# Kernel optimization log

Hardware: AMD Instinct MI355X
Metric: run time of the kernel (lower is better)

Reference implementation:

```python
import jax, jax.numpy as jnp
import numpy as np

B, C_IN, H, W = 32, 128, 64, 64
C_OUT, KH, KW = 256, 3, 3


def setup_inputs() -> dict:
    key = jax.random.key(0)
    k1, k2, k3 = jax.random.split(key, 3)
    inputs = jax.random.normal(k1, (B, C_IN, H, W), dtype=jnp.float32)
    weights = jax.random.normal(k2, (C_OUT, C_IN, KH, KW), dtype=jnp.float32) * 0.05
    bias = jax.random.normal(k3, (C_OUT, 1), dtype=jnp.float32)
    return {"inputs": inputs, "weights": weights, "bias": bias}


def reference(inputs, weights, bias):
    # Direct 2D valid convolution, stride 1, padding 0 (module default).
    # output[b,o,i,j] = sum_{c,u,v} inputs[b,c,i+u,j+v] * weights[o,c,u,v] + bias[o]
    out = jax.lax.conv_general_dilated(
        inputs, weights,
        window_strides=(1, 1),
        padding="VALID",
        dimension_numbers=("NCHW", "OIHW", "NCHW"),
    )
    # bias has shape (C_out, 1); broadcast per output channel
    return out + bias.reshape(1, -1, 1, 1)
```

## Files before the change

kernel.cpp:

```cpp
#include <hip/hip_runtime.h>
#include <hip/hip_bf16.h>
#include <stdint.h>

#define BB   32
#define CIN  128
#define HH   64
#define WW   64
#define COUT 256
#define OHH  62
#define OWW  62
#define PIX_PER_B (OHH*OWW)
#define NPIX (BB*PIX_PER_B)
#define KTOT (9*CIN)

typedef __bf16 bf16x8 __attribute__((ext_vector_type(8)));
typedef float  f32x4  __attribute__((ext_vector_type(4)));
typedef uint16_t u16x8 __attribute__((ext_vector_type(8)));

__device__ __forceinline__ uint16_t f2bf(float f) {
    uint32_t u = __float_as_uint(f);
    uint32_t r = (u + 0x7FFFu + ((u >> 16) & 1u)) >> 16;
    return (uint16_t)r;
}

__device__ __forceinline__ void gload_lds16(const void* g, void* l) {
    __builtin_amdgcn_global_load_lds(
        (const __attribute__((address_space(1))) uint32_t*)g,
        (__attribute__((address_space(3))) uint32_t*)l, 16, 0, 0);
}

__global__ void __launch_bounds__(256) to_nhwc(const float* __restrict__ in,
                                               uint16_t* __restrict__ out) {
    int slab = blockIdx.x;
    int b = slab >> 6, h = slab & 63;
    int w  = threadIdx.x & 63;
    int cp = threadIdx.x >> 6;
    const float* src = in + (((size_t)b * CIN) * HH + h) * WW + w;
    uint16_t* dst = out + ((size_t)slab * WW + w) * CIN;
    #pragma unroll
    for (int it = 0; it < 4; ++it) {
        int c0 = cp * 32 + it * 8;
        u16x8 v;
        #pragma unroll
        for (int j = 0; j < 8; ++j) v[j] = f2bf(src[(c0 + j) * (HH * WW)]);
        *reinterpret_cast<u16x8*>(dst + c0) = v;
    }
}

__global__ void __launch_bounds__(256) pack_w(const float* __restrict__ w,
                                              uint16_t* __restrict__ out) {
    int idx = blockIdx.x * 256 + threadIdx.x;
    int o = idx / KTOT;
    int k = idx - o * KTOT;
    int uv = k >> 7, c = k & 127;
    out[idx] = f2bf(w[(o * CIN + c) * 9 + uv]);
}

__global__ void __launch_bounds__(256) conv_mfma(
        const uint16_t* __restrict__ Xg,
        const uint16_t* __restrict__ Wg,
        const float*    __restrict__ bias,
        float*          __restrict__ out)
{
    __shared__ char lds[32 * 1024 + 1024];
    char* Alds = lds;
    char* Xlds = lds + 16 * 1024;
    int*  pbase = (int*)(lds + 32 * 1024);
    int*  obase = (int*)(lds + 32 * 1024 + 512);

    const int tid  = threadIdx.x;
    const int lane = tid & 63;
    const int wid  = tid >> 6;
    const int bid  = blockIdx.x;
    const int mt = bid & 1;
    const int nt = bid >> 1;

    if (tid < 128) {
        int n  = nt * 128 + tid;
        int b  = n / PIX_PER_B;
        int rem = n - b * PIX_PER_B;
        int oh = rem / OWW;
        int ow = rem - oh * OWW;
        pbase[tid] = ((b * 64 + oh) * 64 + ow) * 128;
        obase[tid] = b * (COUT * PIX_PER_B) + rem;
    }
    __syncthreads();

    const int kc = ((lane & 7) ^ ((lane >> 3) & 7)) * 16;
    int xrow_off[4];
    int arow_off[4];
    #pragma unroll
    for (int q = 0; q < 4; ++q) {
        int t   = wid * 4 + q;
        int row = t * 8 + (lane >> 3);
        xrow_off[q] = pbase[row];
        arow_off[q] = (mt * 128 + row) * KTOT;
    }

    f32x4 acc[4][4] = {};
    const char* XgB = (const char*)Xg;
    const char* WgB = (const char*)Wg;
    const int wm = wid >> 1, wn = wid & 1;

    for (int uv = 0; uv < 9; ++uv) {
        int u = uv / 3, v = uv - u * 3;
        int ioff = (u * 64 + v) * 128;
        #pragma unroll
        for (int ch = 0; ch < 2; ++ch) {
            int c0   = ch * 64;
            int koff = uv * 128 + c0;
            #pragma unroll
            for (int q = 0; q < 4; ++q) {
                int t = wid * 4 + q;
                gload_lds16(WgB + 2 * (arow_off[q] + koff) + kc,
                            Alds + t * 1024 + lane * 16);
                gload_lds16(XgB + 2 * (xrow_off[q] + ioff + c0) + kc,
                            Xlds + t * 1024 + lane * 16);
            }
            __syncthreads();
            #pragma unroll
            for (int ks = 0; ks < 2; ++ks) {
                bf16x8 af[4], xf[4];
                #pragma unroll
                for (int mi = 0; mi < 4; ++mi) {
                    int row = wm * 64 + mi * 16 + (lane & 15);
                    int by  = row * 128 +
                              ((ks * 64 + (lane >> 4) * 16) ^ ((row & 7) << 4));
                    af[mi] = *reinterpret_cast<const bf16x8*>(Alds + by);
                }
                #pragma unroll
                for (int nj = 0; nj < 4; ++nj) {
                    int row = wn * 64 + nj * 16 + (lane & 15);
                    int by  = row * 128 +
                              ((ks * 64 + (lane >> 4) * 16) ^ ((row & 7) << 4));
                    xf[nj] = *reinterpret_cast<const bf16x8*>(Xlds + by);
                }
                #pragma unroll
                for (int mi = 0; mi < 4; ++mi)
                    #pragma unroll
                    for (int nj = 0; nj < 4; ++nj)
                        acc[mi][nj] = __builtin_amdgcn_mfma_f32_16x16x32_bf16(
                            af[mi], xf[nj], acc[mi][nj], 0, 0, 0);
            }
            __syncthreads();
        }
    }

    #pragma unroll
    for (int mi = 0; mi < 4; ++mi) {
        int o = mt * 128 + wm * 64 + mi * 16 + (lane >> 4) * 4;
        #pragma unroll
        for (int reg = 0; reg < 4; ++reg) {
            float bv = bias[o + reg];
            #pragma unroll
            for (int nj = 0; nj < 4; ++nj) {
                int pl  = wn * 64 + nj * 16 + (lane & 15);
                int off = obase[pl] + (o + reg) * PIX_PER_B;
                out[off] = acc[mi][nj][reg] + bv;
            }
        }
    }
}

__global__ void __launch_bounds__(256) conv_naive(const float* __restrict__ in,
                                                  const float* __restrict__ w,
                                                  const float* __restrict__ bias,
                                                  float* __restrict__ out) {
    long idx = (long)blockIdx.x * 256 + threadIdx.x;
    int t = (int)idx;
    int ow = t % OWW; t /= OWW;
    int oh = t % OHH; t /= OHH;
    int o  = t % COUT;
    int b  = t / COUT;
    float s = bias[o];
    for (int c = 0; c < CIN; ++c)
        for (int u = 0; u < 3; ++u)
            for (int v = 0; v < 3; ++v)
                s += in[((b * CIN + c) * HH + oh + u) * WW + ow + v] *
                     w[((o * CIN + c) * 3 + u) * 3 + v];
    out[idx] = s;
}

extern "C" void kernel_launch(void* const* d_in, const int* in_sizes, int n_in,
                              void* d_out, int out_size, void* d_ws, size_t ws_size,
                              hipStream_t stream) {
    const float* in   = (const float*)d_in[0];
    const float* wt   = (const float*)d_in[1];
    const float* bias = (const float*)d_in[2];
    float* out = (float*)d_out;

    const size_t xg_elems = (size_t)BB * HH * WW * CIN;
    const size_t wg_elems = (size_t)COUT * KTOT;
    const size_t need = (xg_elems + wg_elems) * sizeof(uint16_t);

    if (ws_size < need) {
        long total = (long)BB * COUT * OHH * OWW;
        conv_naive<<<(int)((total + 255) / 256), 256, 0, stream>>>(in, wt, bias, out);
        return;
    }

    uint16_t* Xg = (uint16_t*)d_ws;
    uint16_t* Wg = Xg + xg_elems;

    to_nhwc<<<BB * HH, 256, 0, stream>>>(in, Xg);
    pack_w<<<(COUT * KTOT) / 256, 256, 0, stream>>>(wt, Wg);
    conv_mfma<<<2 * (NPIX / 128), 256, 0, stream>>>(Xg, Wg, bias, out);
}
```

Baseline: 120.1 us.

## Pipeline conv GEMM with triple-buffered LDS, full-COUT tiles and XCD-aware block mapping

Replaces the 256-thread, 128x128-tile conv kernel with a 512-thread kernel where each block computes all 256 output channels for 128 pixels. This removes the duplicated input-tile loads across the two M tiles. Global-to-LDS loads now use a three-slot ring buffer, staging chunk k+2 while MFMAs run on chunk k, with explicit vmcnt waits, barriers and s_setprio around the MFMA bursts. Block IDs are remapped so each XCD works on a contiguous range of pixel tiles for cache locality. The cost is a large LDS footprint (about 145KB), which limits residency to one block per CU, and a more fragile hand-written waitcnt schedule.

```diff
diff --git a/kernel.cpp b/kernel.cpp
--- a/kernel.cpp
+++ b/kernel.cpp
@@ -12,6 +12,8 @@
 #define PIX_PER_B (OHH*OWW)
 #define NPIX (BB*PIX_PER_B)
 #define KTOT (9*CIN)
+#define NKT  18
+#define SLOT_BYTES 49152
 
 typedef __bf16 bf16x8 __attribute__((ext_vector_type(8)));
 typedef float  f32x4  __attribute__((ext_vector_type(4)));
@@ -56,107 +58,141 @@
     out[idx] = f2bf(w[(o * CIN + c) * 9 + uv]);
 }
 
-__global__ void __launch_bounds__(256) conv_mfma(
+__global__ void __launch_bounds__(512, 2) conv_mfma8(
         const uint16_t* __restrict__ Xg,
         const uint16_t* __restrict__ Wg,
         const float*    __restrict__ bias,
         float*          __restrict__ out)
 {
-    __shared__ char lds[32 * 1024 + 1024];
-    char* Alds = lds;
-    char* Xlds = lds + 16 * 1024;
-    int*  pbase = (int*)(lds + 32 * 1024);
-    int*  obase = (int*)(lds + 32 * 1024 + 512);
+    __shared__ char lds[3 * SLOT_BYTES + 1024];
+    int* pbase = (int*)(lds + 3 * SLOT_BYTES);
+    int* obase = pbase + 128;
 
     const int tid  = threadIdx.x;
     const int lane = tid & 63;
     const int wid  = tid >> 6;
-    const int bid  = blockIdx.x;
-    const int mt = bid & 1;
-    const int nt = bid >> 1;
+
+    int bid = blockIdx.x;
+    int xcd = bid & 7, lid = bid >> 3;
+    int nt  = (xcd == 0 ? 0 : 121 + (xcd - 1) * 120) + lid;
 
     if (tid < 128) {
-        int n  = nt * 128 + tid;
-        int b  = n / PIX_PER_B;
+        int n   = nt * 128 + tid;
+        int b   = n / PIX_PER_B;
         int rem = n - b * PIX_PER_B;
-        int oh = rem / OWW;
-        int ow = rem - oh * OWW;
+        int oh  = rem / OWW;
+        int ow  = rem - oh * OWW;
         pbase[tid] = ((b * 64 + oh) * 64 + ow) * 128;
         obase[tid] = b * (COUT * PIX_PER_B) + rem;
     }
     __syncthreads();
 
-    const int kc = ((lane & 7) ^ ((lane >> 3) & 7)) * 16;
-    int xrow_off[4];
-    int arow_off[4];
-    #pragma unroll
-    for (int q = 0; q < 4; ++q) {
-        int t   = wid * 4 + q;
-        int row = t * 8 + (lane >> 3);
-        xrow_off[q] = pbase[row];
-        arow_off[q] = (mt * 128 + row) * KTOT;
+    const int row8 = tid >> 3;
+    const int ch   = tid & 7;
+    const int kc   = ((ch ^ (row8 & 7)) << 4);
+    const char* WgB = (const char*)Wg;
+    const char* XgB = (const char*)Xg;
+    int aoff[4], xoff[2];
+    #pragma unroll
+    for (int j = 0; j < 4; ++j) aoff[j] = (j * 64 + row8) * (KTOT * 2);
+    #pragma unroll
+    for (int j = 0; j < 2; ++j) xoff[j] = pbase[j * 64 + row8] * 2;
+    const int ldst = tid * 16;
+
+    auto stage_half = [&](int k, char* sbase, int h) {
+        int uvv = k >> 1;
+        int u   = uvv / 3, v = uvv - u * 3;
+        int c0b = (k & 1) * 128;
+        int wk  = uvv * 256 + c0b;
+        int xk  = (u * 64 + v) * 256 + c0b;
+        char* A = sbase;
+        char* X = sbase + 32768;
+        if (h == 0) {
+            gload_lds16(WgB + (aoff[0] + wk + kc), A + 0 * 8192 + ldst);
+            gload_lds16(WgB + (aoff[1] + wk + kc), A + 1 * 8192 + ldst);
+            gload_lds16(XgB + (xoff[0] + xk + kc), X + 0 * 8192 + ldst);
+        } else {
+            gload_lds16(WgB + (aoff[2] + wk + kc), A + 2 * 8192 + ldst);
+            gload_lds16(WgB + (aoff[3] + wk + kc), A + 3 * 8192 + ldst);
+            gload_lds16(XgB + (xoff[1] + xk + kc), X + 1 * 8192 + ldst);
+        }
+    };
+
+    const int wm = wid >> 1, wn = wid & 1;
+    int aro[4][2], xro[4][2];
+    #pragma unroll
+    for (int mi = 0; mi < 4; ++mi) {
+        int row = wm * 64 + mi * 16 + (lane & 15);
+        #pragma unroll
+        for (int ks = 0; ks < 2; ++ks)
+            aro[mi][ks] = row * 128 +
+                ((ks * 64 + (lane >> 4) * 16) ^ ((row & 7) << 4));
+    }
+    #pragma unroll
+    for (int nj = 0; nj < 4; ++nj) {
+        int row = wn * 64 + nj * 16 + (lane & 15);
+        #pragma unroll
+        for (int ks = 0; ks < 2; ++ks)
+            xro[nj][ks] = 32768 + row * 128 +
+                ((ks * 64 + (lane >> 4) * 16) ^ ((row & 7) << 4));
     }
 
     f32x4 acc[4][4] = {};
-    const char* XgB = (const char*)Xg;
-    const char* WgB = (const char*)Wg;
-    const int wm = wid >> 1, wn = wid & 1;
-
-    for (int uv = 0; uv < 9; ++uv) {
-        int u = uv / 3, v = uv - u * 3;
-        int ioff = (u * 64 + v) * 128;
-        #pragma unroll
-        for (int ch = 0; ch < 2; ++ch) {
-            int c0   = ch * 64;
-            int koff = uv * 128 + c0;
-            #pragma unroll
-            for (int q = 0; q < 4; ++q) {
-                int t = wid * 4 + q;
-                gload_lds16(WgB + 2 * (arow_off[q] + koff) + kc,
-                            Alds + t * 1024 + lane * 16);
-                gload_lds16(XgB + 2 * (xrow_off[q] + ioff + c0) + kc,
-                            Xlds + t * 1024 + lane * 16);
+
+    stage_half(0, lds + 0 * SLOT_BYTES, 0);
+    stage_half(0, lds + 0 * SLOT_BYTES, 1);
+    stage_half(1, lds + 1 * SLOT_BYTES, 0);
+    stage_half(1, lds + 1 * SLOT_BYTES, 1);
+    asm volatile("s_waitcnt vmcnt(6)" ::: "memory");
+    __builtin_amdgcn_s_barrier();
+
+    int s = 0, s2 = 2;
+    for (int kt = 0; kt < NKT; ++kt) {
+        char* sb  = lds + s  * SLOT_BYTES;
+        char* sb2 = lds + s2 * SLOT_BYTES;
+        #pragma unroll
+        for (int ks = 0; ks < 2; ++ks) {
+            bf16x8 af[4], xf[4];
+            #pragma unroll
+            for (int mi = 0; mi < 4; ++mi)
+                af[mi] = *reinterpret_cast<const bf16x8*>(sb + aro[mi][ks]);
+            #pragma unroll
+            for (int nj = 0; nj < 4; ++nj)
+                xf[nj] = *reinterpret_cast<const bf16x8*>(sb + xro[nj][ks]);
+            if (kt < NKT - 2) stage_half(kt + 2, sb2, ks);
+            __builtin_amdgcn_s_barrier();
+            __builtin_amdgcn_s_setprio(1);
+            #pragma unroll
+            for (int mi = 0; mi < 4; ++mi)
+                #pragma unroll
+                for (int nj = 0; nj < 4; ++nj)
+                    acc[mi][nj] = __builtin_amdgcn_mfma_f32_16x16x32_bf16(
+                        af[mi], xf[nj], acc[mi][nj], 0, 0, 0);
+            __builtin_amdgcn_s_setprio(0);
+            if (ks == 0) {
+                __builtin_amdgcn_s_barrier();
+            } else {
+                if (kt < NKT - 2)
+                    asm volatile("s_waitcnt vmcnt(6)" ::: "memory");
+                else if (kt == NKT - 2)
+                    asm volatile("s_waitcnt vmcnt(0)" ::: "memory");
+                __builtin_amdgcn_s_barrier();
             }
-            __syncthreads();
-            #pragma unroll
-            for (int ks = 0; ks < 2; ++ks) {
-                bf16x8 af[4], xf[4];
-                #pragma unroll
-                for (int mi = 0; mi < 4; ++mi) {
-                    int row = wm * 64 + mi * 16 + (lane & 15);
-                    int by  = row * 128 +
-                              ((ks * 64 + (lane >> 4) * 16) ^ ((row & 7) << 4));
-                    af[mi] = *reinterpret_cast<const bf16x8*>(Alds + by);
-                }
-                #pragma unroll
-                for (int nj = 0; nj < 4; ++nj) {
-                    int row = wn * 64 + nj * 16 + (lane & 15);
-                    int by  = row * 128 +
-                              ((ks * 64 + (lane >> 4) * 16) ^ ((row & 7) << 4));
-                    xf[nj] = *reinterpret_cast<const bf16x8*>(Xlds + by);
-                }
-                #pragma unroll
-                for (int mi = 0; mi < 4; ++mi)
-                    #pragma unroll
-                    for (int nj = 0; nj < 4; ++nj)
-                        acc[mi][nj] = __builtin_amdgcn_mfma_f32_16x16x32_bf16(
-                            af[mi], xf[nj], acc[mi][nj], 0, 0, 0);
-            }
-            __syncthreads();
         }
+        s  = (s  == 2) ? 0 : s  + 1;
+        s2 = (s2 == 2) ? 0 : s2 + 1;
     }
 
     #pragma unroll
     for (int mi = 0; mi < 4; ++mi) {
-        int o = mt * 128 + wm * 64 + mi * 16 + (lane >> 4) * 4;
+        int o = wm * 64 + mi * 16 + ((lane >> 4) << 2);
         #pragma unroll
         for (int reg = 0; reg < 4; ++reg) {
             float bv = bias[o + reg];
             #pragma unroll
             for (int nj = 0; nj < 4; ++nj) {
-                int pl  = wn * 64 + nj * 16 + (lane & 15);
-                int off = obase[pl] + (o + reg) * PIX_PER_B;
-                out[off] = acc[mi][nj][reg] + bv;
+                int pl = wn * 64 + nj * 16 + (lane & 15);
+                out[obase[pl] + (o + reg) * PIX_PER_B] = acc[mi][nj][reg] + bv;
             }
         }
     }
@@ -204,5 +240,5 @@
 
     to_nhwc<<<BB * HH, 256, 0, stream>>>(in, Xg);
     pack_w<<<(COUT * KTOT) / 256, 256, 0, stream>>>(wt, Wg);
-    conv_mfma<<<2 * (NPIX / 128), 256, 0, stream>>>(Xg, Wg, bias, out);
-}
+    conv_mfma8<<<NPIX / 128, 512, 0, stream>>>(Xg, Wg, bias, out);
+}
```

Measured after the change: 117.0 us. 2.6% less time.

## Rewrite conv GEMM as 256x256-tile, 8-wave, double-buffered pipelined MFMA kernel

Applied to the files above, without the earlier changes.

Replaces the 128x128 tile conv kernel with a 512-thread kernel that computes a full 256-channel by 256-pixel tile, so input pixels are loaded once instead of twice across two M tiles. LDS is double-buffered (128 KB) with staged global-to-LDS loads interleaved into MFMA phases using manual barriers, waitcnt and setprio to overlap memory and compute. Blocks are remapped by XCD so neighbouring pixel tiles share an L2, and tail pixels are masked. The large LDS footprint and 128 accumulator registers per lane limit occupancy, and the hand-written barrier and waitcnt schedule is fragile.

```diff
diff --git a/kernel.cpp b/kernel.cpp
--- a/kernel.cpp
+++ b/kernel.cpp
@@ -12,6 +12,8 @@
 #define PIX_PER_B (OHH*OWW)
 #define NPIX (BB*PIX_PER_B)
 #define KTOT (9*CIN)
+#define NKT  18
+#define NTBLK 481
 
 typedef __bf16 bf16x8 __attribute__((ext_vector_type(8)));
 typedef float  f32x4  __attribute__((ext_vector_type(4)));
@@ -56,107 +58,140 @@
     out[idx] = f2bf(w[(o * CIN + c) * 9 + uv]);
 }
 
-__global__ void __launch_bounds__(256) conv_mfma(
+__global__ void __launch_bounds__(512, 2) conv_mfma8(
         const uint16_t* __restrict__ Xg,
         const uint16_t* __restrict__ Wg,
         const float*    __restrict__ bias,
         float*          __restrict__ out)
 {
-    __shared__ char lds[32 * 1024 + 1024];
-    char* Alds = lds;
-    char* Xlds = lds + 16 * 1024;
-    int*  pbase = (int*)(lds + 32 * 1024);
-    int*  obase = (int*)(lds + 32 * 1024 + 512);
+    __shared__ char lds[131072 + 2048];
+    int* pbase = (int*)(lds + 131072);
+    int* obase = pbase + 256;
 
     const int tid  = threadIdx.x;
     const int lane = tid & 63;
     const int wid  = tid >> 6;
-    const int bid  = blockIdx.x;
-    const int mt = bid & 1;
-    const int nt = bid >> 1;
-
-    if (tid < 128) {
-        int n  = nt * 128 + tid;
-        int b  = n / PIX_PER_B;
-        int rem = n - b * PIX_PER_B;
-        int oh = rem / OWW;
-        int ow = rem - oh * OWW;
+
+    int bid = blockIdx.x;
+    int xcd = bid & 7, lid = bid >> 3;
+    int nt  = (xcd == 0 ? lid : 61 + (xcd - 1) * 60 + lid);
+
+    if (tid < 256) {
+        int n     = nt * 256 + tid;
+        int valid = n < NPIX;
+        int nn    = valid ? n : NPIX - 1;
+        int b     = nn / PIX_PER_B;
+        int rem   = nn - b * PIX_PER_B;
+        int oh    = rem / OWW;
+        int ow    = rem - oh * OWW;
         pbase[tid] = ((b * 64 + oh) * 64 + ow) * 128;
-        obase[tid] = b * (COUT * PIX_PER_B) + rem;
+        obase[tid] = valid ? b * (COUT * PIX_PER_B) + rem : -1;
     }
     __syncthreads();
 
-    const int kc = ((lane & 7) ^ ((lane >> 3) & 7)) * 16;
-    int xrow_off[4];
-    int arow_off[4];
-    #pragma unroll
-    for (int q = 0; q < 4; ++q) {
-        int t   = wid * 4 + q;
-        int row = t * 8 + (lane >> 3);
-        xrow_off[q] = pbase[row];
-        arow_off[q] = (mt * 128 + row) * KTOT;
-    }
-
-    f32x4 acc[4][4] = {};
+    const int cs   = (((tid & 3) ^ ((tid >> 3) & 3)) << 4);
+    const int ldst = tid * 16;
+    const char* WgB = (const char*)Wg;
     const char* XgB = (const char*)Xg;
-    const char* WgB = (const char*)Wg;
-    const int wm = wid >> 1, wn = wid & 1;
-
-    for (int uv = 0; uv < 9; ++uv) {
-        int u = uv / 3, v = uv - u * 3;
-        int ioff = (u * 64 + v) * 128;
+    int aow[2], pxw[2];
+    aow[0] = (tid >> 2) * (KTOT * 2);
+    aow[1] = (128 + (tid >> 2)) * (KTOT * 2);
+    pxw[0] = pbase[tid >> 2] * 2;
+    pxw[1] = pbase[128 + (tid >> 2)] * 2;
+
+    auto stage = [&](int t, int kh, int op) {
+        if (t >= NKT) return;
+        char* region = lds + (t & 1) * 65536 + kh * 32768 + op * 16384;
+        int uvv = t >> 1;
+        int u   = (uvv * 11) >> 5;
+        int v   = uvv - u * 3;
+        int kb  = ((t & 1) << 7) + (kh << 6) + cs;
+        if (op == 0) {
+            int kf = uvv * 256 + kb;
+            gload_lds16(WgB + aow[0] + kf, region + ldst);
+            gload_lds16(WgB + aow[1] + kf, region + 8192 + ldst);
+        } else {
+            int kf = (u * 64 + v) * 256 + kb;
+            gload_lds16(XgB + pxw[0] + kf, region + ldst);
+            gload_lds16(XgB + pxw[1] + kf, region + 8192 + ldst);
+        }
+    };
+
+    const int wm = wid >> 2, wn = wid & 3;
+    int aoff_frag[8], xoff_frag[4];
+    #pragma unroll
+    for (int a = 0; a < 2; ++a)
         #pragma unroll
-        for (int ch = 0; ch < 2; ++ch) {
-            int c0   = ch * 64;
-            int koff = uv * 128 + c0;
-            #pragma unroll
-            for (int q = 0; q < 4; ++q) {
-                int t = wid * 4 + q;
-                gload_lds16(WgB + 2 * (arow_off[q] + koff) + kc,
-                            Alds + t * 1024 + lane * 16);
-                gload_lds16(XgB + 2 * (xrow_off[q] + ioff + c0) + kc,
-                            Xlds + t * 1024 + lane * 16);
-            }
-            __syncthreads();
-            #pragma unroll
-            for (int ks = 0; ks < 2; ++ks) {
-                bf16x8 af[4], xf[4];
-                #pragma unroll
-                for (int mi = 0; mi < 4; ++mi) {
-                    int row = wm * 64 + mi * 16 + (lane & 15);
-                    int by  = row * 128 +
-                              ((ks * 64 + (lane >> 4) * 16) ^ ((row & 7) << 4));
-                    af[mi] = *reinterpret_cast<const bf16x8*>(Alds + by);
-                }
-                #pragma unroll
-                for (int nj = 0; nj < 4; ++nj) {
-                    int row = wn * 64 + nj * 16 + (lane & 15);
-                    int by  = row * 128 +
-                              ((ks * 64 + (lane >> 4) * 16) ^ ((row & 7) << 4));
-                    xf[nj] = *reinterpret_cast<const bf16x8*>(Xlds + by);
-                }
-                #pragma unroll
-                for (int mi = 0; mi < 4; ++mi)
-                    #pragma unroll
-                    for (int nj = 0; nj < 4; ++nj)
-                        acc[mi][nj] = __builtin_amdgcn_mfma_f32_16x16x32_bf16(
-                            af[mi], xf[nj], acc[mi][nj], 0, 0, 0);
-            }
-            __syncthreads();
+        for (int mi = 0; mi < 4; ++mi) {
+            int row = wm * 128 + a * 64 + mi * 16 + (lane & 15);
+            aoff_frag[a * 4 + mi] = row * 64 +
+                ((((lane >> 4) ^ ((row >> 1) & 3))) << 4);
         }
-    }
-
-    #pragma unroll
-    for (int mi = 0; mi < 4; ++mi) {
-        int o = mt * 128 + wm * 64 + mi * 16 + (lane >> 4) * 4;
+    #pragma unroll
+    for (int nj = 0; nj < 4; ++nj) {
+        int row = wn * 64 + nj * 16 + (lane & 15);
+        xoff_frag[nj] = row * 64 + ((((lane >> 4) ^ ((row >> 1) & 3))) << 4);
+    }
+
+    f32x4 acc[8][4] = {};
+    bf16x8 xf[4];
+    char* bA = lds;
+    char* bB = lds + 65536;
+
+#define PHASE(BUFC, A, KS, RX, ST, SKH, SOP, VMC) do {                         \
+    char* _kb = (BUFC) + (KS) * 32768;                                         \
+    if (RX) { _Pragma("unroll") for (int nj = 0; nj < 4; ++nj)                 \
+        xf[nj] = *reinterpret_cast<const bf16x8*>(_kb + 16384 + xoff_frag[nj]); } \
+    bf16x8 af[4];                                                              \
+    _Pragma("unroll") for (int mi = 0; mi < 4; ++mi)                           \
+        af[mi] = *reinterpret_cast<const bf16x8*>(_kb + aoff_frag[(A)*4+mi]);  \
+    stage((ST), (SKH), (SOP));                                                 \
+    __builtin_amdgcn_s_barrier();                                              \
+    asm volatile("s_waitcnt lgkmcnt(0)" ::: "memory");                         \
+    __builtin_amdgcn_sched_barrier(0);                                         \
+    __builtin_amdgcn_s_setprio(1);                                             \
+    _Pragma("unroll") for (int mi = 0; mi < 4; ++mi)                           \
+      _Pragma("unroll") for (int nj = 0; nj < 4; ++nj)                         \
+        acc[(A)*4+mi][nj] = __builtin_amdgcn_mfma_f32_16x16x32_bf16(           \
+            af[mi], xf[nj], acc[(A)*4+mi][nj], 0, 0, 0);                       \
+    __builtin_amdgcn_s_setprio(0);                                             \
+    if ((VMC) == 1) asm volatile("s_waitcnt vmcnt(4)" ::: "memory");           \
+    else if ((VMC) == 2) asm volatile("s_waitcnt vmcnt(0)" ::: "memory");      \
+    __builtin_amdgcn_s_barrier();                                              \
+    if (VMC) __builtin_amdgcn_sched_barrier(0);                                \
+} while (0)
+
+    stage(0, 0, 0); stage(0, 0, 1);
+    stage(0, 1, 0); stage(0, 1, 1);
+    stage(1, 0, 0); stage(1, 0, 1);
+    asm volatile("s_waitcnt vmcnt(4)" ::: "memory");
+    __builtin_amdgcn_s_barrier();
+
+    for (int i = 0; i < 9; ++i) {
+        const int t = 2 * i;
+        const int vm = (i == 8) ? 2 : 1;
+        PHASE(bA, 0, 0, 1, t + 1, 1, 0, 0);
+        PHASE(bA, 1, 0, 0, t + 1, 1, 1, 0);
+        PHASE(bA, 0, 1, 1, t + 2, 0, 0, 0);
+        PHASE(bA, 1, 1, 0, t + 2, 0, 1, vm);
+        PHASE(bB, 0, 0, 1, t + 2, 1, 0, 0);
+        PHASE(bB, 1, 0, 0, t + 2, 1, 1, 0);
+        PHASE(bB, 0, 1, 1, t + 3, 0, 0, 0);
+        PHASE(bB, 1, 1, 0, t + 3, 0, 1, vm);
+    }
+#undef PHASE
+
+    #pragma unroll
+    for (int mi = 0; mi < 8; ++mi) {
+        int o = wm * 128 + mi * 16 + ((lane >> 4) << 2);
         #pragma unroll
         for (int reg = 0; reg < 4; ++reg) {
             float bv = bias[o + reg];
             #pragma unroll
             for (int nj = 0; nj < 4; ++nj) {
-                int pl  = wn * 64 + nj * 16 + (lane & 15);
-                int off = obase[pl] + (o + reg) * PIX_PER_B;
-                out[off] = acc[mi][nj][reg] + bv;
+                int pl = wn * 64 + nj * 16 + (lane & 15);
+                int ob = obase[pl];
+                if (ob >= 0) out[ob + (o + reg) * PIX_PER_B] = acc[mi][nj][reg] + bv;
             }
         }
     }
@@ -204,5 +239,5 @@
 
     to_nhwc<<<BB * HH, 256, 0, stream>>>(in, Xg);
     pack_w<<<(COUT * KTOT) / 256, 256, 0, stream>>>(wt, Wg);
-    conv_mfma<<<2 * (NPIX / 128), 256, 0, stream>>>(Xg, Wg, bias, out);
-}
+    conv_mfma8<<<NTBLK, 512, 0, stream>>>(Xg, Wg, bias, out);
+}
```

Result: no change. 120.2 us (+0.1%).
